# Kernel optimization log

Measured on AMD Instinct MI355X. Metric: run time of the kernel, lower is better.

Reference implementation:

```python
import jax, jax.numpy as jnp
import numpy as np

B, H, S, DK = 2, 16, 2048, 64


def setup_inputs() -> dict:
    key = jax.random.key(0)
    kq, kk, kv = jax.random.split(key, 3)
    q = jax.random.normal(kq, (B, H, S, DK), dtype=jnp.float32)
    k = jax.random.normal(kk, (B, H, S, DK), dtype=jnp.float32)
    v = jax.random.normal(kv, (B, H, S, DK), dtype=jnp.float32)
    # 3-D boolean mask [B, Sq, Sk]; True = allowed. Causal lower-triangular.
    mask = jnp.broadcast_to(jnp.tril(jnp.ones((S, S), dtype=bool)), (B, S, S))
    return {"q": q, "k": k, "v": v, "mask": mask}


def reference(q, k, v, mask):
    # scores: [B, H, Sq, Sk]
    scores = jnp.einsum("bhqd,bhkd->bhqk", q, k) / jnp.sqrt(jnp.asarray(DK, q.dtype))
    if mask.ndim == scores.ndim - 1:
        mask = mask[:, None, :, :]  # broadcast over heads
    scores = jnp.where(mask, scores, jnp.asarray(-jnp.inf, scores.dtype))
    attn = jax.nn.softmax(scores, axis=-1)
    out = jnp.einsum("bhqk,bhkd->bhqd", attn, v)
    return out
```

## Files before the change

kernel.cpp:

```cpp
#include <hip/hip_runtime.h>


typedef float    v4f __attribute__((ext_vector_type(4)));
typedef _Float16 v4h __attribute__((ext_vector_type(4)));
typedef _Float16 v8h __attribute__((ext_vector_type(8)));

#define SEQ 2048
#define DKC 64

#if __has_builtin(__builtin_amdgcn_exp2f)
#define EXP2(x) __builtin_amdgcn_exp2f(x)
#else
#define EXP2(x) exp2f(x)
#endif

#define MFMA16(a,b,c) __builtin_amdgcn_mfma_f32_16x16x16f16(a,b,c,0,0,0)
#define MFMA32(a,b,c) __builtin_amdgcn_mfma_f32_16x16x32_f16(a,b,c,0,0,0)

__global__ __launch_bounds__(256) void prep_kv(const float* __restrict__ k,
                                               const float* __restrict__ v,
                                               _Float16* __restrict__ kh,
                                               _Float16* __restrict__ vt) {
  const int bh = blockIdx.x;
  const int kt = blockIdx.y;
  const int tid = threadIdx.x;
  {
    const int quad = tid & 3;
    const int l16  = (tid >> 2) & 15;
    const int st   = (tid >> 6) & 1;
    const int s    = tid >> 7;
    const float* src = k + ((size_t)bh * SEQ + kt * 32 + s * 16 + l16) * DKC + st * 32 + quad * 8;
    float4 a = *(const float4*)src;
    float4 b = *(const float4*)(src + 4);
    v8h h;
    h[0] = (_Float16)a.x; h[1] = (_Float16)a.y; h[2] = (_Float16)a.z; h[3] = (_Float16)a.w;
    h[4] = (_Float16)b.x; h[5] = (_Float16)b.y; h[6] = (_Float16)b.z; h[7] = (_Float16)b.w;
    *(v8h*)(kh + (size_t)bh * SEQ * DKC
               + (size_t)(kt * 4 + s * 2 + st) * 512 + (quad * 16 + l16) * 8) = h;
  }
  {
    const int d = tid & 63, q4 = tid >> 6;
    const float* src = v + ((size_t)bh * SEQ + kt * 32) * DKC + d;
    v8h h;
#pragma unroll
    for (int j = 0; j < 4; ++j) h[j]     = (_Float16)src[(size_t)(q4 * 4 + j) * DKC];
#pragma unroll
    for (int j = 0; j < 4; ++j) h[4 + j] = (_Float16)src[(size_t)(16 + q4 * 4 + j) * DKC];
    *(v8h*)(vt + (size_t)bh * SEQ * DKC + (size_t)kt * 2048
               + (d >> 4) * 512 + (q4 * 16 + (d & 15)) * 8) = h;
  }
}

__device__ __forceinline__ void compute_chunk(int k0, bool straddle, int qw, int l16, int quad,
                                              const v8h (&qf)[2][2],
                                              const v8h (&kf)[4], const v8h (&va)[4],
                                              v4f (&O)[2][4], v4f (&L)[2], const v4h ones) {
  v4f S[2][2] = {};
#pragma unroll
  for (int t = 0; t < 2; ++t)
#pragma unroll
    for (int s = 0; s < 2; ++s) {
      S[t][s] = MFMA32(kf[s * 2 + 0], qf[t][0], S[t][s]);
      S[t][s] = MFMA32(kf[s * 2 + 1], qf[t][1], S[t][s]);
    }

  if (straddle) {
#pragma unroll
    for (int t = 0; t < 2; ++t) {
      const int qg = qw + t * 16 + l16;
#pragma unroll
      for (int s = 0; s < 2; ++s) {
        const int kb = k0 + s * 16 + quad * 4;
#pragma unroll
        for (int r = 0; r < 4; ++r)
          if (kb + r > qg) S[t][s][r] = -3e38f;
      }
    }
  }

  v4h pf[2][2];
#pragma unroll
  for (int t = 0; t < 2; ++t)
#pragma unroll
    for (int s = 0; s < 2; ++s) {
      v4h p;
#pragma unroll
      for (int r = 0; r < 4; ++r) p[r] = (_Float16)EXP2(S[t][s][r]);
      pf[t][s] = p;
    }

#pragma unroll
  for (int dc = 0; dc < 4; ++dc) {
    v4h lo = __builtin_shufflevector(va[dc], va[dc], 0, 1, 2, 3);
    v4h hi = __builtin_shufflevector(va[dc], va[dc], 4, 5, 6, 7);
    O[0][dc] = MFMA16(lo, pf[0][0], O[0][dc]);
    O[0][dc] = MFMA16(hi, pf[0][1], O[0][dc]);
    O[1][dc] = MFMA16(lo, pf[1][0], O[1][dc]);
    O[1][dc] = MFMA16(hi, pf[1][1], O[1][dc]);
  }
  L[0] = MFMA16(ones, pf[0][0], L[0]);
  L[0] = MFMA16(ones, pf[0][1], L[0]);
  L[1] = MFMA16(ones, pf[1][0], L[1]);
  L[1] = MFMA16(ones, pf[1][1], L[1]);
}

#define GLD16(gp, lp) __builtin_amdgcn_global_load_lds(                     \
    (const __attribute__((address_space(1))) void*)(gp),                    \
    (__attribute__((address_space(3))) void*)(lp), 16, 0, 0)

#define STAGE(bf, c) do {                                                   \
    const char* _gk = khb + (size_t)(c) * 16384 + w * 4096 + lane * 16;     \
    const char* _gv = vtb + (size_t)(c) * 16384 + w * 4096 + lane * 16;     \
    char* _lk = ((char*)&lds[bf][0][0]) + w * 4096;                         \
    char* _lv = ((char*)&lds[bf][1][0]) + w * 4096;                         \
    GLD16(_gk,        _lk);        GLD16(_gk + 1024, _lk + 1024);           \
    GLD16(_gk + 2048, _lk + 2048); GLD16(_gk + 3072, _lk + 3072);           \
    GLD16(_gv,        _lv);        GLD16(_gv + 1024, _lv + 1024);           \
    GLD16(_gv + 2048, _lv + 2048); GLD16(_gv + 3072, _lv + 3072);           \
  } while (0)

__global__ __launch_bounds__(256) void fa_fwd(const float* __restrict__ q,
                                              const _Float16* __restrict__ kh,
                                              const _Float16* __restrict__ vt,
                                              float* __restrict__ out) {
  __shared__ _Float16 lds[2][2][8192];

  const int lane = threadIdx.x & 63;
  const int w    = threadIdx.x >> 6;
  const int quad = lane >> 4;
  const int l16  = lane & 15;

  const int g  = (int)blockIdx.x & 7;
  const int r  = (int)blockIdx.x >> 3;
  const int bh = g * 4 + (r & 3);
  const int p  = r >> 2;
  const int qb = (p < 8) ? p : (23 - p);

  const size_t base = (size_t)bh * SEQ * DKC;
  const char* khb = (const char*)(kh + base);
  const char* vtb = (const char*)(vt + base);

  const float CSC = 0.18033688011112042f;
  const v4h ones = {(_Float16)1.f, (_Float16)1.f, (_Float16)1.f, (_Float16)1.f};

  const int qw  = qb * 128 + w * 32;
  const int myk = qb * 4 + w;
  const int NC  = qb + 1;

  v8h qf[2][2];
#pragma unroll
  for (int t = 0; t < 2; ++t)
#pragma unroll
    for (int st = 0; st < 2; ++st) {
      const float* qr = q + base + (size_t)(qw + t * 16 + l16) * DKC + st * 32 + quad * 8;
      float4 a = *(const float4*)qr;
      float4 b = *(const float4*)(qr + 4);
      v8h hq;
      hq[0] = (_Float16)(a.x * CSC); hq[1] = (_Float16)(a.y * CSC);
      hq[2] = (_Float16)(a.z * CSC); hq[3] = (_Float16)(a.w * CSC);
      hq[4] = (_Float16)(b.x * CSC); hq[5] = (_Float16)(b.y * CSC);
      hq[6] = (_Float16)(b.z * CSC); hq[7] = (_Float16)(b.w * CSC);
      qf[t][st] = hq;
    }

  v4f O[2][4] = {};
  v4f L[2]    = {};

  STAGE(0, 0);
  __syncthreads();

  for (int c = 0; c < NC; ++c) {
    if (c + 1 < NC) STAGE((c + 1) & 1, c + 1);
    const int b = c & 1;
#pragma unroll
    for (int kl = 0; kl < 4; ++kl) {
      const int kt32 = c * 4 + kl;
      if (kt32 <= myk) {
        v8h kf[4], va[4];
#pragma unroll
        for (int i = 0; i < 4; ++i) kf[i] = *(const v8h*)&lds[b][0][kl * 2048 + i * 512 + lane * 8];
#pragma unroll
        for (int i = 0; i < 4; ++i) va[i] = *(const v8h*)&lds[b][1][kl * 2048 + i * 512 + lane * 8];
        compute_chunk(kt32 * 32, kt32 == myk, qw, l16, quad, qf, kf, va, O, L, ones);
      }
    }
    __syncthreads();
  }

#pragma unroll
  for (int t = 0; t < 2; ++t) {
    const float inv = 1.0f / L[t][0];
    float* orow = out + base + (size_t)(qw + t * 16 + l16) * DKC + quad * 4;
#pragma unroll
    for (int dc = 0; dc < 4; ++dc) {
      float4 o;
      o.x = O[t][dc][0] * inv; o.y = O[t][dc][1] * inv;
      o.z = O[t][dc][2] * inv; o.w = O[t][dc][3] * inv;
      *(float4*)(orow + dc * 16) = o;
    }
  }
}

extern "C" void kernel_launch(void* const* d_in, const int* in_sizes, int n_in,
                              void* d_out, int out_size, void* d_ws, size_t ws_size,
                              hipStream_t stream) {
  (void)in_sizes; (void)n_in; (void)out_size; (void)ws_size;
  const float* q = (const float*)d_in[0];
  const float* k = (const float*)d_in[1];
  const float* v = (const float*)d_in[2];
  float* out = (float*)d_out;

  _Float16* kh = (_Float16*)d_ws;
  _Float16* vt = (_Float16*)((char*)d_ws + (size_t)32 * SEQ * DKC * 2);

  prep_kv<<<dim3(32, 64), dim3(256), 0, stream>>>(k, v, kh, vt);
  fa_fwd<<<dim3(512), dim3(256), 0, stream>>>(q, kh, vt, out);
}
```

Before: 143.4 us.

## Pair complementary causal query blocks per workgroup and split key tiles across wave groups

```diff
diff --git a/kernel.cpp b/kernel.cpp
--- a/kernel.cpp
+++ b/kernel.cpp
@@ -109,24 +109,24 @@
     (__attribute__((address_space(3))) void*)(lp), 16, 0, 0)
 
 #define STAGE(bf, c) do {                                                   \
-    const char* _gk = khb + (size_t)(c) * 16384 + w * 4096 + lane * 16;     \
-    const char* _gv = vtb + (size_t)(c) * 16384 + w * 4096 + lane * 16;     \
-    char* _lk = ((char*)&lds[bf][0][0]) + w * 4096;                         \
-    char* _lv = ((char*)&lds[bf][1][0]) + w * 4096;                         \
-    GLD16(_gk,        _lk);        GLD16(_gk + 1024, _lk + 1024);           \
-    GLD16(_gk + 2048, _lk + 2048); GLD16(_gk + 3072, _lk + 3072);           \
-    GLD16(_gv,        _lv);        GLD16(_gv + 1024, _lv + 1024);           \
-    GLD16(_gv + 2048, _lv + 2048); GLD16(_gv + 3072, _lv + 3072);           \
+    const char* _gk = khb + (size_t)(c) * 16384 + wv * 2048 + lane * 16;    \
+    const char* _gv = vtb + (size_t)(c) * 16384 + wv * 2048 + lane * 16;    \
+    char* _lk = ((char*)&lds[bf][0][0]) + wv * 2048;                        \
+    char* _lv = ((char*)&lds[bf][1][0]) + wv * 2048;                        \
+    GLD16(_gk, _lk); GLD16(_gk + 1024, _lk + 1024);                         \
+    GLD16(_gv, _lv); GLD16(_gv + 1024, _lv + 1024);                         \
   } while (0)
 
-__global__ __launch_bounds__(256) void fa_fwd(const float* __restrict__ q,
+__global__ __launch_bounds__(512) void fa_fwd(const float* __restrict__ q,
                                               const _Float16* __restrict__ kh,
                                               const _Float16* __restrict__ vt,
                                               float* __restrict__ out) {
   __shared__ _Float16 lds[2][2][8192];
 
   const int lane = threadIdx.x & 63;
-  const int w    = threadIdx.x >> 6;
+  const int wv   = threadIdx.x >> 6;
+  const int w    = wv & 3;
+  const int grp  = wv >> 2;
   const int quad = lane >> 4;
   const int l16  = lane & 15;
 
@@ -134,7 +134,6 @@
   const int r  = (int)blockIdx.x >> 3;
   const int bh = g * 4 + (r & 3);
   const int p  = r >> 2;
-  const int qb = (p < 8) ? p : (23 - p);
 
   const size_t base = (size_t)bh * SEQ * DKC;
   const char* khb = (const char*)(kh + base);
@@ -143,28 +142,38 @@
   const float CSC = 0.18033688011112042f;
   const v4h ones = {(_Float16)1.f, (_Float16)1.f, (_Float16)1.f, (_Float16)1.f};
 
-  const int qw  = qb * 128 + w * 32;
-  const int myk = qb * 4 + w;
-  const int NC  = qb + 1;
-
-  v8h qf[2][2];
+  const int qwA  = p * 128 + w * 32;
+  const int qwB  = (15 - p) * 128 + w * 32;
+  const int mykA = 4 * p + w;
+  const int mykB = 4 * (15 - p) + w;
+  const int NC   = 16 - p;
+
+  v8h qfA[2][2], qfB[2][2];
 #pragma unroll
   for (int t = 0; t < 2; ++t)
 #pragma unroll
     for (int st = 0; st < 2; ++st) {
-      const float* qr = q + base + (size_t)(qw + t * 16 + l16) * DKC + st * 32 + quad * 8;
-      float4 a = *(const float4*)qr;
-      float4 b = *(const float4*)(qr + 4);
+      const float* qrA = q + base + (size_t)(qwA + t * 16 + l16) * DKC + st * 32 + quad * 8;
+      const float* qrB = q + base + (size_t)(qwB + t * 16 + l16) * DKC + st * 32 + quad * 8;
+      float4 a = *(const float4*)qrA;
+      float4 b = *(const float4*)(qrA + 4);
       v8h hq;
       hq[0] = (_Float16)(a.x * CSC); hq[1] = (_Float16)(a.y * CSC);
       hq[2] = (_Float16)(a.z * CSC); hq[3] = (_Float16)(a.w * CSC);
       hq[4] = (_Float16)(b.x * CSC); hq[5] = (_Float16)(b.y * CSC);
       hq[6] = (_Float16)(b.z * CSC); hq[7] = (_Float16)(b.w * CSC);
-      qf[t][st] = hq;
-    }
-
-  v4f O[2][4] = {};
-  v4f L[2]    = {};
+      qfA[t][st] = hq;
+      a = *(const float4*)qrB;
+      b = *(const float4*)(qrB + 4);
+      hq[0] = (_Float16)(a.x * CSC); hq[1] = (_Float16)(a.y * CSC);
+      hq[2] = (_Float16)(a.z * CSC); hq[3] = (_Float16)(a.w * CSC);
+      hq[4] = (_Float16)(b.x * CSC); hq[5] = (_Float16)(b.y * CSC);
+      hq[6] = (_Float16)(b.z * CSC); hq[7] = (_Float16)(b.w * CSC);
+      qfB[t][st] = hq;
+    }
+
+  v4f OA[2][4] = {}, OB[2][4] = {};
+  v4f LA[2] = {}, LB[2] = {};
 
   STAGE(0, 0);
   __syncthreads();
@@ -174,29 +183,82 @@
     const int b = c & 1;
 #pragma unroll
     for (int kl = 0; kl < 4; ++kl) {
+      if ((kl & 1) != grp) continue;
       const int kt32 = c * 4 + kl;
-      if (kt32 <= myk) {
+      if (kt32 <= mykB) {
         v8h kf[4], va[4];
 #pragma unroll
         for (int i = 0; i < 4; ++i) kf[i] = *(const v8h*)&lds[b][0][kl * 2048 + i * 512 + lane * 8];
 #pragma unroll
         for (int i = 0; i < 4; ++i) va[i] = *(const v8h*)&lds[b][1][kl * 2048 + i * 512 + lane * 8];
-        compute_chunk(kt32 * 32, kt32 == myk, qw, l16, quad, qf, kf, va, O, L, ones);
+        if (kt32 <= mykA)
+          compute_chunk(kt32 * 32, kt32 == mykA, qwA, l16, quad, qfA, kf, va, OA, LA, ones);
+        compute_chunk(kt32 * 32, kt32 == mykB, qwB, l16, quad, qfB, kf, va, OB, LB, ones);
       }
     }
     __syncthreads();
   }
 
-#pragma unroll
-  for (int t = 0; t < 2; ++t) {
-    const float inv = 1.0f / L[t][0];
-    float* orow = out + base + (size_t)(qw + t * 16 + l16) * DKC + quad * 4;
-#pragma unroll
-    for (int dc = 0; dc < 4; ++dc) {
-      float4 o;
-      o.x = O[t][dc][0] * inv; o.y = O[t][dc][1] * inv;
-      o.z = O[t][dc][2] * inv; o.w = O[t][dc][3] * inv;
-      *(float4*)(orow + dc * 16) = o;
+  v4f (*cb)[64] = (v4f(*)[64])&lds[0][0][0];
+
+  if (!grp) {
+#pragma unroll
+    for (int t = 0; t < 2; ++t) {
+#pragma unroll
+      for (int dc = 0; dc < 4; ++dc) cb[w * 10 + t * 4 + dc][lane] = OA[t][dc];
+      cb[w * 10 + 8 + t][lane] = LA[t];
+    }
+  }
+  __syncthreads();
+  if (grp) {
+#pragma unroll
+    for (int t = 0; t < 2; ++t) {
+#pragma unroll
+      for (int dc = 0; dc < 4; ++dc) OA[t][dc] += cb[w * 10 + t * 4 + dc][lane];
+      LA[t] += cb[w * 10 + 8 + t][lane];
+    }
+#pragma unroll
+    for (int t = 0; t < 2; ++t) {
+      const float inv = 1.0f / LA[t][0];
+      float* orow = out + base + (size_t)(qwA + t * 16 + l16) * DKC + quad * 4;
+#pragma unroll
+      for (int dc = 0; dc < 4; ++dc) {
+        float4 o;
+        o.x = OA[t][dc][0] * inv; o.y = OA[t][dc][1] * inv;
+        o.z = OA[t][dc][2] * inv; o.w = OA[t][dc][3] * inv;
+        *(float4*)(orow + dc * 16) = o;
+      }
+    }
+  }
+  __syncthreads();
+
+  if (grp) {
+#pragma unroll
+    for (int t = 0; t < 2; ++t) {
+#pragma unroll
+      for (int dc = 0; dc < 4; ++dc) cb[w * 10 + t * 4 + dc][lane] = OB[t][dc];
+      cb[w * 10 + 8 + t][lane] = LB[t];
+    }
+  }
+  __syncthreads();
+  if (!grp) {
+#pragma unroll
+    for (int t = 0; t < 2; ++t) {
+#pragma unroll
+      for (int dc = 0; dc < 4; ++dc) OB[t][dc] += cb[w * 10 + t * 4 + dc][lane];
+      LB[t] += cb[w * 10 + 8 + t][lane];
+    }
+#pragma unroll
+    for (int t = 0; t < 2; ++t) {
+      const float inv = 1.0f / LB[t][0];
+      float* orow = out + base + (size_t)(qwB + t * 16 + l16) * DKC + quad * 4;
+#pragma unroll
+      for (int dc = 0; dc < 4; ++dc) {
+        float4 o;
+        o.x = OB[t][dc][0] * inv; o.y = OB[t][dc][1] * inv;
+        o.z = OB[t][dc][2] * inv; o.w = OB[t][dc][3] * inv;
+        *(float4*)(orow + dc * 16) = o;
+      }
     }
   }
 }
@@ -214,5 +276,5 @@
   _Float16* vt = (_Float16*)((char*)d_ws + (size_t)32 * SEQ * DKC * 2);
 
   prep_kv<<<dim3(32, 64), dim3(256), 0, stream>>>(k, v, kh, vt);
-  fa_fwd<<<dim3(512), dim3(256), 0, stream>>>(q, kh, vt, out);
-}
+  fa_fwd<<<dim3(256), dim3(512), 0, stream>>>(q, kh, vt, out);
+}
```

Result: faster. 137.3 us (-4.2%).
